# Performance work log

Measured on AMD Instinct MI355X. Metric: run time of the kernel, lower is better.

The kernel has to match this reference:

```python
import jax, jax.numpy as jnp
import numpy as np

COMMITMENT_COST = 0.25
TEMP = 0.1

def _normalize(x):
    # matches F.normalize(dim=-1): x / max(||x||, 1e-12)
    return x / jnp.maximum(jnp.linalg.norm(x, axis=-1, keepdims=True), 1e-12)

def setup_inputs() -> dict:
    key = jax.random.key(0)
    k1, k2 = jax.random.split(key)
    B, T, D, K = 16, 1024, 256, 4096
    inputs = jax.random.normal(k1, (B, T, D), dtype=jnp.float32)
    # embedding initialized N(0,1) then L2-normalized, as in __init__
    codebook = _normalize(jax.random.normal(k2, (K, D), dtype=jnp.float32))
    return {"inputs": inputs, "codebook": codebook}

def reference(inputs, codebook):
    K, D = codebook.shape
    flat = inputs.reshape(-1, D)                      # [N, D]
    flat_n = _normalize(flat)                         # [N, D]
    cb_n = jax.lax.stop_gradient(_normalize(codebook))  # [K, D] (weight.detach())
    # squared cosine distance: 2 - 2 * <x, e>
    dist = 2.0 - 2.0 * jnp.matmul(flat_n, cb_n.T)     # [N, K]
    soft_probs = jax.nn.softmax(-dist / TEMP, axis=1)  # [N, K]
    idx = jnp.argmin(dist, axis=1)                    # [N]
    # one-hot @ codebook == gather
    quantized = cb_n[idx].reshape(inputs.shape)       # [B, T, D]
    x_n = flat_n.reshape(inputs.shape)
    e_latent_loss = jnp.mean((jax.lax.stop_gradient(quantized) - x_n) ** 2)
    vq_loss = COMMITMENT_COST * e_latent_loss
    # straight-through estimator
    quant_st = x_n + jax.lax.stop_gradient(quantized - x_n)
    # perplexity from hard assignment histogram
    counts = jnp.zeros((K,), dtype=flat.dtype).at[idx].add(1.0)
    avg_probs = counts / flat.shape[0]
    perplexity = jnp.exp(-jnp.sum(avg_probs * jnp.log(avg_probs + 1e-10)))
    return vq_loss, quant_st, soft_probs, perplexity, idx[:, None]
```

## Files before the change

kernel.cpp:

```cpp
#include <hip/hip_runtime.h>
#include <cstdint>
#include <cstddef>

#define D_DIM 256
#define K_CODES 4096
#define N_ROWS 16384
#define NORM_ROWS_PER_BLK 32

typedef __attribute__((ext_vector_type(4))) int   i32x4;
typedef __attribute__((ext_vector_type(4))) float f32x4;

__device__ __forceinline__ unsigned short f2bf(float x) {
    const unsigned int u = __float_as_uint(x);
    return (unsigned short)((u + 0x7fffu + ((u >> 16) & 1u)) >> 16);
}
__device__ __forceinline__ float bf2f(unsigned short h) {
    return __uint_as_float((unsigned int)h << 16);
}

__device__ __forceinline__ void gload16(const unsigned short* g, unsigned short* l) {
    __builtin_amdgcn_global_load_lds(
        (const __attribute__((address_space(1))) void*)g,
        (__attribute__((address_space(3))) void*)l, 16, 0, 0);
}

#define MFMA(c, a, b) \
    asm volatile("v_mfma_f32_16x16x32_bf16 %0, %1, %2, %0" : "+v"(c) : "v"(a), "v"(b))

__device__ __forceinline__ float np_sumsq_128(const float* __restrict__ a)
{
    float r[8];
    #pragma unroll
    for (int j = 0; j < 8; ++j) r[j] = __fmul_rn(a[j], a[j]);
    #pragma unroll
    for (int i = 8; i < 128; i += 8)
        #pragma unroll
        for (int j = 0; j < 8; ++j)
            r[j] = __fadd_rn(r[j], __fmul_rn(a[i + j], a[i + j]));
    return __fadd_rn(__fadd_rn(__fadd_rn(r[0], r[1]), __fadd_rn(r[2], r[3])),
                     __fadd_rn(__fadd_rn(r[4], r[5]), __fadd_rn(r[6], r[7])));
}

__global__ __launch_bounds__(256) void norm_rows_np_kernel(
    const float* __restrict__ src, float* __restrict__ dst,
    unsigned short* __restrict__ dsth, unsigned short* __restrict__ dstl)
{
    __shared__ float lds[NORM_ROWS_PER_BLK * D_DIM];
    __shared__ float nrm[NORM_ROWS_PER_BLK];
    const int tid = threadIdx.x;
    const size_t base = (size_t)blockIdx.x * NORM_ROWS_PER_BLK * D_DIM;

    #pragma unroll
    for (int i = 0; i < NORM_ROWS_PER_BLK; ++i)
        lds[i * 256 + tid] = src[base + i * 256 + tid];
    __syncthreads();

    if (tid < NORM_ROWS_PER_BLK) {
        const float* row = &lds[tid * D_DIM];
        const float tot = __fadd_rn(np_sumsq_128(row), np_sumsq_128(row + 128));
        const float n = (float)sqrt((double)tot);
        nrm[tid] = fmaxf(n, 1e-12f);
    }
    __syncthreads();

    #pragma unroll
    for (int i = 0; i < NORM_ROWS_PER_BLK; ++i) {
        const int e = i * 256 + tid;
        const float v = lds[e] / nrm[i];
        dst[base + e] = v;
        const unsigned short h = f2bf(v);
        dsth[base + e] = h;
        dstl[base + e] = f2bf(v - bf2f(h));
    }
}

__global__ __launch_bounds__(256) void gemm_bf16x3_kernel(
    const unsigned short* __restrict__ Ah, const unsigned short* __restrict__ Al,
    const unsigned short* __restrict__ Bh, const unsigned short* __restrict__ Bl,
    float* __restrict__ C)
{
    __shared__ __align__(16) unsigned short smem[2 * 4 * 4096];

    const int tid  = threadIdx.x;
    const int lane = tid & 63;
    const int wv   = tid >> 6;
    const int wr   = wv >> 1, wc = wv & 1;

    const int GX  = K_CODES / 128;
    const int lin = blockIdx.y * GX + blockIdx.x;
    const int swz = (lin & 7) * (4096 / 8) + (lin >> 3);
    const int bm  = (swz / GX) * 128;
    const int bn  = (swz % GX) * 128;

    const int og0 = tid, og1 = 256 + tid;
    const int row0 = og0 >> 2, row1 = og1 >> 2;
    const int g0 = (og0 & 3) ^ ((row0 >> 1) & 3);
    const int g1 = (og1 & 3) ^ ((row1 >> 1) & 3);
    const size_t asrc0 = (size_t)(bm + row0) * D_DIM + g0 * 8;
    const size_t asrc1 = (size_t)(bm + row1) * D_DIM + g1 * 8;
    const size_t bsrc0 = (size_t)(bn + row0) * D_DIM + g0 * 8;
    const size_t bsrc1 = (size_t)(bn + row1) * D_DIM + g1 * 8;

    int aoff[4], boff[4];
    #pragma unroll
    for (int i = 0; i < 4; ++i) {
        const int ar = wr * 64 + i * 16 + (lane & 15);
        aoff[i] = ar * 64 + ((((lane >> 4) ^ ((ar >> 1) & 3)) & 3) << 4);
        const int br = wc * 64 + i * 16 + (lane & 15);
        boff[i] = br * 64 + ((((lane >> 4) ^ ((br >> 1) & 3)) & 3) << 4);
    }
    const char* sA = (const char*)smem;

    auto stage = [&](int buf, int k0) {
        unsigned short* l0 = smem + buf * 16384 + wv * 512;
        unsigned short* l1 = smem + buf * 16384 + 2048 + wv * 512;
        gload16(Ah + asrc0 + k0, l0);
        gload16(Ah + asrc1 + k0, l1);
        gload16(Al + asrc0 + k0, l0 + 4096);
        gload16(Al + asrc1 + k0, l1 + 4096);
        gload16(Bh + bsrc0 + k0, l0 + 8192);
        gload16(Bh + bsrc1 + k0, l1 + 8192);
        gload16(Bl + bsrc0 + k0, l0 + 12288);
        gload16(Bl + bsrc1 + k0, l1 + 12288);
    };

    f32x4 acc[4][4] = {};

    stage(0, 0);
    stage(1, 32);

    #pragma unroll
    for (int t = 0; t < 8; ++t) {
        const int b = t & 1;
        if (t < 7) asm volatile("s_waitcnt vmcnt(8)" ::: "memory");
        else       asm volatile("s_waitcnt vmcnt(0)" ::: "memory");
        __builtin_amdgcn_s_barrier();
        __builtin_amdgcn_sched_barrier(0);

        const char* base = sA + b * 32768;
        i32x4 ah[4], al[4], bh[4], bl[4];
        #pragma unroll
        for (int i = 0; i < 4; ++i) {
            ah[i] = *(const i32x4*)(base +         aoff[i]);
            al[i] = *(const i32x4*)(base +  8192 + aoff[i]);
            bh[i] = *(const i32x4*)(base + 16384 + boff[i]);
            bl[i] = *(const i32x4*)(base + 24576 + boff[i]);
        }
        #pragma unroll
        for (int i = 0; i < 4; ++i)
            #pragma unroll
            for (int j = 0; j < 4; ++j)
                MFMA(acc[i][j], ah[i], bh[j]);
        #pragma unroll
        for (int i = 0; i < 4; ++i)
            #pragma unroll
            for (int j = 0; j < 4; ++j)
                MFMA(acc[i][j], ah[i], bl[j]);
        #pragma unroll
        for (int i = 0; i < 4; ++i)
            #pragma unroll
            for (int j = 0; j < 4; ++j)
                MFMA(acc[i][j], al[i], bh[j]);

        __builtin_amdgcn_sched_barrier(0);
        __builtin_amdgcn_s_barrier();
        __builtin_amdgcn_sched_barrier(0);

        if (t < 6) stage(b, (t + 2) * 32);
    }
    asm volatile("s_nop 7\n\ts_nop 7\n\ts_nop 7");

    #pragma unroll
    for (int i = 0; i < 4; ++i) {
        const int r0 = bm + wr * 64 + i * 16 + ((lane >> 4) << 2);
        #pragma unroll
        for (int j = 0; j < 4; ++j) {
            const int c0 = bn + wc * 64 + j * 16 + (lane & 15);
            #pragma unroll
            for (int r = 0; r < 4; ++r)
                C[(size_t)(r0 + r) * K_CODES + c0] = acc[i][j][r];
        }
    }
}

__global__ __launch_bounds__(256) void rowpass_kernel(
    float* __restrict__ P,
    const float* __restrict__ cbn,
    float* __restrict__ xq,
    float* __restrict__ idx_out,
    float* __restrict__ counts,
    float* __restrict__ rowloss)
{
    const int w = threadIdx.x >> 6;
    const int l = threadIdx.x & 63;
    const int row = blockIdx.x * 4 + w;
    float4* rp = (float4*)(P + (size_t)row * K_CODES);

    __shared__ float s_x[4][D_DIM];
    __shared__ int   s_cand[4][128];
    __shared__ int   s_cnt[4];

    float vals[64];
    #pragma unroll
    for (int j = 0; j < 16; ++j) {
        const float4 v = rp[j * 64 + l];
        vals[j * 4 + 0] = v.x; vals[j * 4 + 1] = v.y;
        vals[j * 4 + 2] = v.z; vals[j * 4 + 3] = v.w;
    }
    const float4 xv4 = *(const float4*)&xq[(size_t)row * D_DIM + l * 4];
    *(float4*)&s_x[w][l * 4] = xv4;
    if (l == 0) s_cnt[w] = 0;

    float m = -1e30f, bd = 3.402823466e+38f;
    #pragma unroll
    for (int i = 0; i < 64; ++i) {
        m  = fmaxf(m, vals[i]);
        bd = fminf(bd, 2.0f - 2.0f * vals[i]);
    }
    #pragma unroll
    for (int off = 32; off > 0; off >>= 1) {
        m  = fmaxf(m,  __shfl_down(m,  off));
        bd = fminf(bd, __shfl_down(bd, off));
    }
    const float M  = __shfl(m, 0);
    const float fb = __shfl(bd, 0);

    const float TAU = 0.0078125f;
    #pragma unroll
    for (int i = 0; i < 64; ++i) {
        const float d = 2.0f - 2.0f * vals[i];
        if (d <= fb + TAU) {
            const int p = atomicAdd(&s_cnt[w], 1);
            if (p < 128) s_cand[w][p] = ((i >> 2) * 64 + l) * 4 + (i & 3);
        }
    }
    const int cnt = min(s_cnt[w], 128);

    int besti;
    if (cnt == 1) {
        besti = s_cand[w][0];
    } else {
        float bdx = 3.402823466e+38f; int bii = 0x7fffffff;
        for (int c = l; c < cnt; c += 64) {
            const int ii = s_cand[w][c];
            const float* cb = cbn + (size_t)ii * D_DIM;
            float a = 0.0f;
            for (int k = 0; k < D_DIM; ++k) a = fmaf(s_x[w][k], cb[k], a);
            const float d = 2.0f - 2.0f * a;
            if (d < bdx || (d == bdx && ii < bii)) { bdx = d; bii = ii; }
        }
        #pragma unroll
        for (int off = 32; off > 0; off >>= 1) {
            const float od = __shfl_down(bdx, off);
            const int   oi = __shfl_down(bii, off);
            if (od < bdx || (od == bdx && oi < bii)) { bdx = od; bii = oi; }
        }
        besti = __shfl(bii, 0);
    }

    float esum = 0.0f;
    #pragma unroll
    for (int i = 0; i < 64; ++i) {
        vals[i] = __expf(20.0f * (vals[i] - M));
        esum += vals[i];
    }
    #pragma unroll
    for (int off = 32; off > 0; off >>= 1) esum += __shfl_down(esum, off);
    const float inv = 1.0f / __shfl(esum, 0);
    #pragma unroll
    for (int j = 0; j < 16; ++j) {
        rp[j * 64 + l] = make_float4(vals[j * 4 + 0] * inv, vals[j * 4 + 1] * inv,
                                     vals[j * 4 + 2] * inv, vals[j * 4 + 3] * inv);
    }

    const float4 q4 = *(const float4*)&cbn[(size_t)besti * D_DIM + l * 4];
    *(float4*)&xq[(size_t)row * D_DIM + l * 4] = q4;
    const float d0 = q4.x - xv4.x, d1 = q4.y - xv4.y;
    const float d2 = q4.z - xv4.z, d3 = q4.w - xv4.w;
    float ls = d0 * d0 + d1 * d1 + d2 * d2 + d3 * d3;
    #pragma unroll
    for (int off = 32; off > 0; off >>= 1) ls += __shfl_down(ls, off);
    if (l == 0) {
        rowloss[row] = ls;
        idx_out[row] = (float)besti;
        atomicAdd(&counts[besti], 1.0f);
    }
}

__global__ __launch_bounds__(256) void finalize_kernel(
    const float* __restrict__ rowloss, const float* __restrict__ counts,
    float* __restrict__ out_loss, float* __restrict__ out_ppl)
{
    const int t = threadIdx.x;
    float s = 0.0f;
    for (int i = t; i < N_ROWS; i += 256) s += rowloss[i];
    float e = 0.0f;
    for (int i = t; i < K_CODES; i += 256) {
        const float avg = counts[i] * (1.0f / (float)N_ROWS);
        e += avg * logf(avg + 1e-10f);
    }
    #pragma unroll
    for (int off = 32; off > 0; off >>= 1) {
        s += __shfl_down(s, off);
        e += __shfl_down(e, off);
    }
    __shared__ float sf[4], se[4];
    if ((t & 63) == 0) { sf[t >> 6] = s; se[t >> 6] = e; }
    __syncthreads();
    if (t == 0) {
        out_loss[0] = 0.25f * (sf[0] + sf[1] + sf[2] + sf[3]) /
                      ((float)N_ROWS * (float)D_DIM);
        out_ppl[0] = expf(-(se[0] + se[1] + se[2] + se[3]));
    }
}

extern "C" void kernel_launch(void* const* d_in, const int* in_sizes, int n_in,
                              void* d_out, int out_size, void* d_ws, size_t ws_size,
                              hipStream_t stream) {
    const float* inputs   = (const float*)d_in[0];
    const float* codebook = (const float*)d_in[1];
    float* out = (float*)d_out;

    float* vq_loss = out;
    float* quant   = out + 1;
    float* probs   = quant + (size_t)N_ROWS * D_DIM;
    float* ppl     = probs + (size_t)N_ROWS * K_CODES;
    float* idxout  = ppl + 1;

    float* cbn     = (float*)d_ws;
    float* counts  = cbn + (size_t)K_CODES * D_DIM;
    float* rowloss = counts + K_CODES;
    unsigned short* Ah = (unsigned short*)(rowloss + N_ROWS);
    unsigned short* Al = Ah + (size_t)N_ROWS * D_DIM;
    unsigned short* Bh = Al + (size_t)N_ROWS * D_DIM;
    unsigned short* Bl = Bh + (size_t)K_CODES * D_DIM;

    hipMemsetAsync(counts, 0, K_CODES * sizeof(float), stream);
    norm_rows_np_kernel<<<K_CODES / NORM_ROWS_PER_BLK, 256, 0, stream>>>(codebook, cbn, Bh, Bl);
    norm_rows_np_kernel<<<N_ROWS / NORM_ROWS_PER_BLK, 256, 0, stream>>>(inputs, quant, Ah, Al);
    gemm_bf16x3_kernel<<<dim3(K_CODES / 128, N_ROWS / 128), 256, 0, stream>>>(Ah, Al, Bh, Bl, probs);
    rowpass_kernel<<<N_ROWS / 4, 256, 0, stream>>>(probs, cbn, quant, idxout, counts, rowloss);
    finalize_kernel<<<1, 256, 0, stream>>>(rowloss, counts, vq_loss, ppl);
}
```

Baseline: 549.0 us.

## Enlarge bf16x3 GEMM tile to 256x256 with 8-wave ping-pong pipelined K loop

Rewrites the codebook-similarity GEMM to use 256x256 tiles with 512 threads, looping over the three bf16 product passes as 12 K-phases of width 64. LDS loads are split into half-tiles issued between MFMA groups, with setprio to raise priority around MFMA bursts. The aim is to raise arithmetic intensity and overlap global loads with compute. It uses 128KB of LDS, which limits occupancy to one block per CU, and adds a more intricate wait-count schedule.

After: 541.0 us. About the same (-1.5%).

```diff
diff --git a/kernel.cpp b/kernel.cpp
--- a/kernel.cpp
+++ b/kernel.cpp
@@ -74,113 +74,146 @@
     }
 }
 
-__global__ __launch_bounds__(256) void gemm_bf16x3_kernel(
+__global__ __launch_bounds__(512, 2) void gemm_bf16x3_kernel(
     const unsigned short* __restrict__ Ah, const unsigned short* __restrict__ Al,
     const unsigned short* __restrict__ Bh, const unsigned short* __restrict__ Bl,
     float* __restrict__ C)
 {
-    __shared__ __align__(16) unsigned short smem[2 * 4 * 4096];
+    __shared__ __align__(16) unsigned short smem[65536];
 
     const int tid  = threadIdx.x;
     const int lane = tid & 63;
     const int wv   = tid >> 6;
-    const int wr   = wv >> 1, wc = wv & 1;
-
-    const int GX  = K_CODES / 128;
+    const int wr   = wv >> 2;
+    const int wc   = wv & 3;
+
+    const int GX  = K_CODES / 256;
     const int lin = blockIdx.y * GX + blockIdx.x;
-    const int swz = (lin & 7) * (4096 / 8) + (lin >> 3);
-    const int bm  = (swz / GX) * 128;
-    const int bn  = (swz % GX) * 128;
-
-    const int og0 = tid, og1 = 256 + tid;
-    const int row0 = og0 >> 2, row1 = og1 >> 2;
-    const int g0 = (og0 & 3) ^ ((row0 >> 1) & 3);
-    const int g1 = (og1 & 3) ^ ((row1 >> 1) & 3);
-    const size_t asrc0 = (size_t)(bm + row0) * D_DIM + g0 * 8;
-    const size_t asrc1 = (size_t)(bm + row1) * D_DIM + g1 * 8;
-    const size_t bsrc0 = (size_t)(bn + row0) * D_DIM + g0 * 8;
-    const size_t bsrc1 = (size_t)(bn + row1) * D_DIM + g1 * 8;
-
-    int aoff[4], boff[4];
-    #pragma unroll
-    for (int i = 0; i < 4; ++i) {
-        const int ar = wr * 64 + i * 16 + (lane & 15);
-        aoff[i] = ar * 64 + ((((lane >> 4) ^ ((ar >> 1) & 3)) & 3) << 4);
-        const int br = wc * 64 + i * 16 + (lane & 15);
-        boff[i] = br * 64 + ((((lane >> 4) ^ ((br >> 1) & 3)) & 3) << 4);
-    }
+    const int swz = (lin & 7) * (1024 / 8) + (lin >> 3);
+    const int bm  = (swz / GX) * 256;
+    const int bn  = (swz % GX) * 256;
+
+    const int srow0 = wv * 32 + (lane >> 2);
+    const int srow1 = srow0 + 16;
+    const int sl    = (lane & 3) ^ ((lane >> 2) & 3);
+
+    #define STAGE_A(T, h)                                                        \
+        do { const unsigned short* pl_ = ((T) < 8) ? Ah : Al;                    \
+             unsigned short* d_ = smem + ((T) & 1) * 32768 + (h) * 8192;         \
+             const int kb_ = ((T) & 3) * 64 + (h) * 32 + sl * 8;                 \
+             gload16(pl_ + (size_t)(bm + srow0) * 256 + kb_, d_ + (wv*2+0)*512); \
+             gload16(pl_ + (size_t)(bm + srow1) * 256 + kb_, d_ + (wv*2+1)*512); \
+        } while (0)
+    #define STAGE_B(T, h)                                                        \
+        do { const unsigned short* pl_ = ((T) < 4) ? Bh : (((T) < 8) ? Bl : Bh); \
+             unsigned short* d_ = smem + ((T) & 1) * 32768 + 16384 + (h) * 8192; \
+             const int kb_ = ((T) & 3) * 64 + (h) * 32 + sl * 8;                 \
+             gload16(pl_ + (size_t)(bn + srow0) * 256 + kb_, d_ + (wv*2+0)*512); \
+             gload16(pl_ + (size_t)(bn + srow1) * 256 + kb_, d_ + (wv*2+1)*512); \
+        } while (0)
+
+    const int fr   = lane & 15;
+    const int phys = ((lane >> 4) ^ (lane & 3));
+    int aoff[8], boff[4];
+    #pragma unroll
+    for (int mi = 0; mi < 8; ++mi)
+        aoff[mi] = (wr * 128 + mi * 16 + fr) * 64 + phys * 16;
+    #pragma unroll
+    for (int ni = 0; ni < 4; ++ni)
+        boff[ni] = 32768 + (wc * 64 + ni * 16 + fr) * 64 + phys * 16;
     const char* sA = (const char*)smem;
 
-    auto stage = [&](int buf, int k0) {
-        unsigned short* l0 = smem + buf * 16384 + wv * 512;
-        unsigned short* l1 = smem + buf * 16384 + 2048 + wv * 512;
-        gload16(Ah + asrc0 + k0, l0);
-        gload16(Ah + asrc1 + k0, l1);
-        gload16(Al + asrc0 + k0, l0 + 4096);
-        gload16(Al + asrc1 + k0, l1 + 4096);
-        gload16(Bh + bsrc0 + k0, l0 + 8192);
-        gload16(Bh + bsrc1 + k0, l1 + 8192);
-        gload16(Bl + bsrc0 + k0, l0 + 12288);
-        gload16(Bl + bsrc1 + k0, l1 + 12288);
-    };
-
-    f32x4 acc[4][4] = {};
-
-    stage(0, 0);
-    stage(1, 32);
-
-    #pragma unroll
-    for (int t = 0; t < 8; ++t) {
-        const int b = t & 1;
-        if (t < 7) asm volatile("s_waitcnt vmcnt(8)" ::: "memory");
-        else       asm volatile("s_waitcnt vmcnt(0)" ::: "memory");
+    f32x4 acc[8][4] = {};
+
+    STAGE_A(0, 0); STAGE_B(0, 0); STAGE_A(0, 1); STAGE_B(0, 1);
+    STAGE_A(1, 0); STAGE_B(1, 0);
+
+    #pragma unroll 2
+    for (int T = 0; T < 12; ++T) {
+        const int buf = T & 1;
+        const char* base0 = sA + buf * 65536;
+        const char* base1 = base0 + 16384;
+        i32x4 a[4], bfr[4];
+
+        if (T < 11) asm volatile("s_waitcnt vmcnt(8)" ::: "memory");
+        else        asm volatile("s_waitcnt vmcnt(4)" ::: "memory");
         __builtin_amdgcn_s_barrier();
         __builtin_amdgcn_sched_barrier(0);
-
-        const char* base = sA + b * 32768;
-        i32x4 ah[4], al[4], bh[4], bl[4];
-        #pragma unroll
-        for (int i = 0; i < 4; ++i) {
-            ah[i] = *(const i32x4*)(base +         aoff[i]);
-            al[i] = *(const i32x4*)(base +  8192 + aoff[i]);
-            bh[i] = *(const i32x4*)(base + 16384 + boff[i]);
-            bl[i] = *(const i32x4*)(base + 24576 + boff[i]);
+        #pragma unroll
+        for (int ni = 0; ni < 4; ++ni) bfr[ni] = *(const i32x4*)(base0 + boff[ni]);
+        #pragma unroll
+        for (int mi = 0; mi < 4; ++mi) a[mi] = *(const i32x4*)(base0 + aoff[mi]);
+        if (T + 1 < 12) STAGE_A(T + 1, 1);
+        asm volatile("s_waitcnt lgkmcnt(0)" ::: "memory");
+        __builtin_amdgcn_sched_barrier(0);
+        __builtin_amdgcn_s_setprio(1);
+        #pragma unroll
+        for (int mi = 0; mi < 4; ++mi)
+            #pragma unroll
+            for (int ni = 0; ni < 4; ++ni) MFMA(acc[mi][ni], a[mi], bfr[ni]);
+        __builtin_amdgcn_s_setprio(0);
+
+        __builtin_amdgcn_s_barrier();
+        __builtin_amdgcn_sched_barrier(0);
+        #pragma unroll
+        for (int mi = 0; mi < 4; ++mi) a[mi] = *(const i32x4*)(base0 + aoff[4 + mi]);
+        if (T + 1 < 12) STAGE_B(T + 1, 1);
+        asm volatile("s_waitcnt lgkmcnt(0)" ::: "memory");
+        __builtin_amdgcn_sched_barrier(0);
+        __builtin_amdgcn_s_setprio(1);
+        #pragma unroll
+        for (int mi = 0; mi < 4; ++mi)
+            #pragma unroll
+            for (int ni = 0; ni < 4; ++ni) MFMA(acc[4 + mi][ni], a[mi], bfr[ni]);
+        __builtin_amdgcn_s_setprio(0);
+
+        if (T < 11) asm volatile("s_waitcnt vmcnt(8)" ::: "memory");
+        else        asm volatile("s_waitcnt vmcnt(0)" ::: "memory");
+        __builtin_amdgcn_s_barrier();
+        __builtin_amdgcn_sched_barrier(0);
+        #pragma unroll
+        for (int ni = 0; ni < 4; ++ni) bfr[ni] = *(const i32x4*)(base1 + boff[ni]);
+        #pragma unroll
+        for (int mi = 0; mi < 4; ++mi) a[mi] = *(const i32x4*)(base1 + aoff[mi]);
+        if (T + 2 < 12) STAGE_A(T + 2, 0);
+        asm volatile("s_waitcnt lgkmcnt(0)" ::: "memory");
+        __builtin_amdgcn_sched_barrier(0);
+        __builtin_amdgcn_s_setprio(1);
+        #pragma unroll
+        for (int mi = 0; mi < 4; ++mi)
+            #pragma unroll
+            for (int ni = 0; ni < 4; ++ni) MFMA(acc[mi][ni], a[mi], bfr[ni]);
+        __builtin_amdgcn_s_setprio(0);
+
+        __builtin_amdgcn_s_barrier();
+        __builtin_amdgcn_sched_barrier(0);
+        #pragma unroll
+        for (int mi = 0; mi < 4; ++mi) a[mi] = *(const i32x4*)(base1 + aoff[4 + mi]);
+        if (T + 2 < 12) STAGE_B(T + 2, 0);
+        asm volatile("s_waitcnt lgkmcnt(0)" ::: "memory");
+        __builtin_amdgcn_sched_barrier(0);
+        __builtin_amdgcn_s_setprio(1);
+        #pragma unroll
+        for (int mi = 0; mi < 4; ++mi)
+            #pragma unroll
+            for (int ni = 0; ni < 4; ++ni) MFMA(acc[4 + mi][ni], a[mi], bfr[ni]);
+        __builtin_amdgcn_s_setprio(0);
+    }
+    asm volatile("s_nop 7\n\ts_nop 7\n\ts_nop 7");
+
+    #pragma unroll
+    for (int mi = 0; mi < 8; ++mi) {
+        const int r0 = bm + wr * 128 + mi * 16 + ((lane >> 4) << 2);
+        #pragma unroll
+        for (int ni = 0; ni < 4; ++ni) {
+            const int c0 = bn + wc * 64 + ni * 16 + (lane & 15);
+            #pragma unroll
+            for (int r = 0; r < 4; ++r)
+                C[(size_t)(r0 + r) * K_CODES + c0] = acc[mi][ni][r];
         }
-        #pragma unroll
-        for (int i = 0; i < 4; ++i)
-            #pragma unroll
-            for (int j = 0; j < 4; ++j)
-                MFMA(acc[i][j], ah[i], bh[j]);
-        #pragma unroll
-        for (int i = 0; i < 4; ++i)
-            #pragma unroll
-            for (int j = 0; j < 4; ++j)
-                MFMA(acc[i][j], ah[i], bl[j]);
-        #pragma unroll
-        for (int i = 0; i < 4; ++i)
-            #pragma unroll
-            for (int j = 0; j < 4; ++j)
-                MFMA(acc[i][j], al[i], bh[j]);
-
-        __builtin_amdgcn_sched_barrier(0);
-        __builtin_amdgcn_s_barrier();
-        __builtin_amdgcn_sched_barrier(0);
-
-        if (t < 6) stage(b, (t + 2) * 32);
-    }
-    asm volatile("s_nop 7\n\ts_nop 7\n\ts_nop 7");
-
-    #pragma unroll
-    for (int i = 0; i < 4; ++i) {
-        const int r0 = bm + wr * 64 + i * 16 + ((lane >> 4) << 2);
-        #pragma unroll
-        for (int j = 0; j < 4; ++j) {
-            const int c0 = bn + wc * 64 + j * 16 + (lane & 15);
-            #pragma unroll
-            for (int r = 0; r < 4; ++r)
-                C[(size_t)(r0 + r) * K_CODES + c0] = acc[i][j][r];
-        }
-    }
+    }
+    #undef STAGE_A
+    #undef STAGE_B
 }
 
 __global__ __launch_bounds__(256) void rowpass_kernel(
@@ -338,7 +371,7 @@
     hipMemsetAsync(counts, 0, K_CODES * sizeof(float), stream);
     norm_rows_np_kernel<<<K_CODES / NORM_ROWS_PER_BLK, 256, 0, stream>>>(codebook, cbn, Bh, Bl);
     norm_rows_np_kernel<<<N_ROWS / NORM_ROWS_PER_BLK, 256, 0, stream>>>(inputs, quant, Ah, Al);
-    gemm_bf16x3_kernel<<<dim3(K_CODES / 128, N_ROWS / 128), 256, 0, stream>>>(Ah, Al, Bh, Bl, probs);
+    gemm_bf16x3_kernel<<<dim3(K_CODES / 256, N_ROWS / 256), 512, 0, stream>>>(Ah, Al, Bh, Bl, probs);
     rowpass_kernel<<<N_ROWS / 4, 256, 0, stream>>>(probs, cbn, quant, idxout, counts, rowloss);
     finalize_kernel<<<1, 256, 0, stream>>>(rowloss, counts, vq_loss, ppl);
 }
```
